# Kernel tuning notes

Hardware: AMD Instinct MI355X
Metric: run time of the kernel (lower is better)

## Reference

```python
import jax, jax.numpy as jnp
import numpy as np

D = 512      # d_model
H = 8        # nhead
HD = D // H  # head dim
L = 8        # axis-0 length (torch seq dim, batch_first=False)
S = 128      # axis-1 length (torch batch dim; relation-tensor axis)
NL = 3       # encoder layers
EPS = 1e-5


def setup_inputs() -> dict:
    key = jax.random.key(0)
    ks = jax.random.split(key, 16)
    w = lambda k, shape: jax.random.normal(k, shape, jnp.float32) * 0.02
    return {
        "x": jax.random.normal(ks[0], (L, S, D), jnp.float32),
        # stacked per-layer transformer params (leading dim = NL)
        "attn_in_w": w(ks[1], (NL, 3 * D, D)), "attn_in_b": jnp.zeros((NL, 3 * D), jnp.float32),
        "attn_out_w": w(ks[2], (NL, D, D)),    "attn_out_b": jnp.zeros((NL, D), jnp.float32),
        "ln1_w": jnp.ones((NL, D), jnp.float32), "ln1_b": jnp.zeros((NL, D), jnp.float32),
        "ln2_w": jnp.ones((NL, D), jnp.float32), "ln2_b": jnp.zeros((NL, D), jnp.float32),
        "ff1_w": w(ks[3], (NL, 4 * D, D)), "ff1_b": jnp.zeros((NL, 4 * D), jnp.float32),
        "ff2_w": w(ks[4], (NL, D, 4 * D)), "ff2_b": jnp.zeros((NL, D), jnp.float32),
        "fln_w": jnp.ones((D,), jnp.float32), "fln_b": jnp.zeros((D,), jnp.float32),
        # 4 projection MLPs stacked: 0=sub, 1=obj, 2=verb_sub, 3=verb_obj
        "mlp_w0": w(ks[5], (4, D, D)), "mlp_b0": jnp.zeros((4, D), jnp.float32),
        "mlp_w1": w(ks[6], (4, D, D)), "mlp_b1": jnp.zeros((4, D), jnp.float32),
        "mlp_w2": w(ks[7], (4, D, D)), "mlp_b2": jnp.zeros((4, D), jnp.float32),
    }


def _ln(x, w, b):
    m = jnp.mean(x, axis=-1, keepdims=True)
    v = jnp.mean(jnp.square(x - m), axis=-1, keepdims=True)
    return (x - m) * jax.lax.rsqrt(v + EPS) * w + b


def _mha(x, in_w, in_b, out_w, out_b):
    # x: (L, B, D); attention over axis 0 (torch batch_first=False semantics)
    l, b, _ = x.shape
    qkv = x @ in_w.T + in_b                      # (L, B, 3D)
    q, k, v = jnp.split(qkv, 3, axis=-1)
    q = q.reshape(l, b, H, HD)
    k = k.reshape(l, b, H, HD)
    v = v.reshape(l, b, H, HD)
    scores = jnp.einsum("lbhd,mbhd->bhlm", q, k) / jnp.sqrt(jnp.float32(HD))
    attn = jax.nn.softmax(scores, axis=-1)
    o = jnp.einsum("bhlm,mbhd->lbhd", attn, v).reshape(l, b, D)
    return o @ out_w.T + out_b


def _mlp(x, w0, b0, w1, b1, w2, b2):
    h = jax.nn.relu(x @ w0.T + b0)
    h = jax.nn.relu(h @ w1.T + b1)
    return h @ w2.T + b2


def _forward(x, attn_in_w, attn_in_b, attn_out_w, attn_out_b,
             ln1_w, ln1_b, ln2_w, ln2_b, ff1_w, ff1_b, ff2_w, ff2_b,
             fln_w, fln_b, mlp_w0, mlp_b0, mlp_w1, mlp_b1, mlp_w2, mlp_b2):
    # TransformerEncoder (post-norm, relu, no dropout at eval)
    h = x
    for i in range(NL):
        h = _ln(h + _mha(h, attn_in_w[i], attn_in_b[i], attn_out_w[i], attn_out_b[i]),
                ln1_w[i], ln1_b[i])
        ff = jax.nn.relu(h @ ff1_w[i].T + ff1_b[i]) @ ff2_w[i].T + ff2_b[i]
        h = _ln(h + ff, ln2_w[i], ln2_b[i])
    h = _ln(h, fln_w, fln_b)  # final encoder norm

    sub = _mlp(h, mlp_w0[0], mlp_b0[0], mlp_w1[0], mlp_b1[0], mlp_w2[0], mlp_b2[0])
    obj = _mlp(h, mlp_w0[1], mlp_b0[1], mlp_w1[1], mlp_b1[1], mlp_w2[1], mlp_b2[1])
    vsub = _mlp(h, mlp_w0[2], mlp_b0[2], mlp_w1[2], mlp_b1[2], mlp_w2[2], mlp_b2[2])
    vobj = _mlp(h, mlp_w0[3], mlp_b0[3], mlp_w1[3], mlp_b1[3], mlp_w2[3], mlp_b2[3])

    # sub.unsqueeze(1) * vsub.unsqueeze(2): (B0, S, S, D)
    sub4 = sub[:, None, :, :] * vsub[:, :, None, :]
    obj4 = obj[:, None, :, :] * vobj[:, :, None, :]
    # p_x = sub4 @ obj4.transpose(-2, -1): (B0, S, S, S)
    return jnp.einsum("bijd,bikd->bijk", sub4, obj4)


def reference(x, attn_in_w, attn_in_b, attn_out_w, attn_out_b,
              ln1_w, ln1_b, ln2_w, ln2_b, ff1_w, ff1_b, ff2_w, ff2_b,
              fln_w, fln_b, mlp_w0, mlp_b0, mlp_w1, mlp_b1, mlp_w2, mlp_b2):
    return _forward(x, attn_in_w, attn_in_b, attn_out_w, attn_out_b,
                    ln1_w, ln1_b, ln2_w, ln2_b, ff1_w, ff1_b, ff2_w, ff2_b,
                    fln_w, fln_b, mlp_w0, mlp_b0, mlp_w1, mlp_b1, mlp_w2, mlp_b2)
```

## Files before the change

### kernel.cpp

```cpp
#include <hip/hip_runtime.h>
#include <hip/hip_bf16.h>

#define DEV __device__ __forceinline__

typedef __attribute__((ext_vector_type(8))) short bf16x8;
typedef __attribute__((ext_vector_type(8))) unsigned short u16x8;
typedef __attribute__((ext_vector_type(4))) float f32x4;

DEV unsigned short f2bf(float f) {
  return __builtin_bit_cast(unsigned short, __float2bfloat16(f));
}
DEV float bf2f(unsigned short h) { return __uint_as_float(((unsigned int)h) << 16); }

DEV int swz(int row, int byteoff) { return row * 128 + (byteoff ^ ((row & 7) << 4)); }

__global__ void cvt_kernel(const float* __restrict__ src, unsigned short* __restrict__ dst,
                           float* __restrict__ dstf, int n) {
  long i = ((long)blockIdx.x * blockDim.x + threadIdx.x) * 8;
  long stride = (long)gridDim.x * blockDim.x * 8;
  for (; i < n; i += stride) {
    f32x4 a = *(const f32x4*)(src + i);
    f32x4 b = *(const f32x4*)(src + i + 4);
    u16x8 o;
    o[0] = f2bf(a[0]); o[1] = f2bf(a[1]); o[2] = f2bf(a[2]); o[3] = f2bf(a[3]);
    o[4] = f2bf(b[0]); o[5] = f2bf(b[1]); o[6] = f2bf(b[2]); o[7] = f2bf(b[3]);
    *(u16x8*)(dst + i) = o;
    if (dstf) { *(f32x4*)(dstf + i) = a; *(f32x4*)(dstf + i + 4) = b; }
  }
}

struct CvtJobs { const float* s[7]; unsigned short* d[7]; int n[7]; };
__global__ void cvtw_kernel(CvtJobs J) {
  const int seg = blockIdx.y;
  const float* __restrict__ src = J.s[seg];
  unsigned short* __restrict__ dst = J.d[seg];
  const int n = J.n[seg];
  long i = ((long)blockIdx.x * blockDim.x + threadIdx.x) * 8;
  long stride = (long)gridDim.x * blockDim.x * 8;
  for (; i < n; i += stride) {
    f32x4 a = *(const f32x4*)(src + i);
    f32x4 b = *(const f32x4*)(src + i + 4);
    u16x8 o;
    o[0] = f2bf(a[0]); o[1] = f2bf(a[1]); o[2] = f2bf(a[2]); o[3] = f2bf(a[3]);
    o[4] = f2bf(b[0]); o[5] = f2bf(b[1]); o[6] = f2bf(b[2]); o[7] = f2bf(b[3]);
    *(u16x8*)(dst + i) = o;
  }
}

template <int BM, int ACT, int WF32, int WBF>
__global__ __launch_bounds__(256) void gemm_kernel(
    const unsigned short* __restrict__ X, const unsigned short* __restrict__ Wt,
    const float* __restrict__ bias, float* Yf, unsigned short* __restrict__ Ybf,
    int M, int N, int K, long xbs, long wbs, long bbs, long ybs) {
  constexpr int CA = (BM * 64) / (256 * 8);
  constexpr int ABY = BM * 64 * 2;
  constexpr int BBY = 64 * 64 * 2;
  constexpr int MI = BM / 32;
  __shared__ __align__(16) char Asb[2 * ABY];
  __shared__ __align__(16) char Bsb[2 * BBY];
  const int t = threadIdx.x;
  const int bn = blockIdx.x, bm = blockIdx.y, bz = blockIdx.z;
  const unsigned short* Xp = X + (long)bz * xbs;
  const unsigned short* Wp = Wt + (long)bz * wbs;

  const int lane = t & 63, wv = t >> 6;
  const int wr = wv >> 1, wc = wv & 1;
  f32x4 acc[MI][2] = {};

  int rowA[CA], slotA[CA], rowB[2], slotB[2];
#pragma unroll
  for (int c = 0; c < CA; ++c) { int id = c * 256 + t; rowA[c] = id >> 3; slotA[c] = id & 7; }
#pragma unroll
  for (int c = 0; c < 2; ++c) { int id = c * 256 + t; rowB[c] = id >> 3; slotB[c] = id & 7; }

  u16x8 ra[CA], rb[2];
  auto load = [&](int kt) {
#pragma unroll
    for (int c = 0; c < CA; ++c)
      ra[c] = *(const u16x8*)(Xp + (long)(bm * BM + rowA[c]) * K + kt + slotA[c] * 8);
#pragma unroll
    for (int c = 0; c < 2; ++c)
      rb[c] = *(const u16x8*)(Wp + (long)(bn * 64 + rowB[c]) * K + kt + slotB[c] * 8);
  };
  auto store = [&](int cur) {
#pragma unroll
    for (int c = 0; c < CA; ++c)
      *(u16x8*)(Asb + cur * ABY + swz(rowA[c], slotA[c] * 16)) = ra[c];
#pragma unroll
    for (int c = 0; c < 2; ++c)
      *(u16x8*)(Bsb + cur * BBY + swz(rowB[c], slotB[c] * 16)) = rb[c];
  };

  const int NT = K >> 6;
  load(0);
  store(0);
  load(64);
  __syncthreads();
  for (int ki = 0; ki < NT; ++ki) {
    const int cur = ki & 1;
    if (ki + 1 < NT) store(cur ^ 1);
    if (ki + 2 < NT) load((ki + 2) << 6);
#pragma unroll
    for (int kk = 0; kk < 2; ++kk) {
      const int kb = kk * 64 + ((lane >> 4) << 4);
      bf16x8 af[MI], bfv[2];
#pragma unroll
      for (int mi = 0; mi < MI; ++mi)
        af[mi] = *(const bf16x8*)(Asb + cur * ABY + swz(wr * (MI * 16) + mi * 16 + (lane & 15), kb));
#pragma unroll
      for (int ni = 0; ni < 2; ++ni)
        bfv[ni] = *(const bf16x8*)(Bsb + cur * BBY + swz(wc * 32 + ni * 16 + (lane & 15), kb));
#pragma unroll
      for (int mi = 0; mi < MI; ++mi)
#pragma unroll
        for (int ni = 0; ni < 2; ++ni)
          acc[mi][ni] = __builtin_amdgcn_mfma_f32_16x16x32_bf16(af[mi], bfv[ni], acc[mi][ni], 0, 0, 0);
    }
    __syncthreads();
  }
#pragma unroll
  for (int ni = 0; ni < 2; ++ni) {
    const int n = bn * 64 + wc * 32 + ni * 16 + (lane & 15);
    const float bv = bias[(long)bz * bbs + n];
#pragma unroll
    for (int mi = 0; mi < MI; ++mi) {
#pragma unroll
      for (int rr = 0; rr < 4; ++rr) {
        const int gm = bm * BM + wr * (MI * 16) + mi * 16 + ((lane >> 4) << 2) + rr;
        float v = acc[mi][ni][rr] + bv;
        if (ACT == 1) v = fmaxf(v, 0.f);
        const long o = (long)bz * ybs + (long)gm * N + n;
        if (WF32) Yf[o] = v;
        if (WBF) Ybf[o] = f2bf(v);
      }
    }
  }
}

__global__ __launch_bounds__(256) void attn_kernel(const unsigned short* __restrict__ qkv,
                                                   unsigned short* __restrict__ o) {
  __shared__ float P[512];
  const int s = blockIdx.x;
  const int t = threadIdx.x;
#pragma unroll
  for (int rep = 0; rep < 2; ++rep) {
    const int idx = t + rep * 256;
    const int h = idx >> 6, l = (idx >> 3) & 7, m = idx & 7;
    const unsigned short* qp = qkv + (long)(l * 128 + s) * 1536 + h * 64;
    const unsigned short* kp = qkv + (long)(m * 128 + s) * 1536 + 512 + h * 64;
    float acc = 0.f;
#pragma unroll
    for (int c = 0; c < 64; c += 8) {
      u16x8 q8 = *(const u16x8*)(qp + c);
      u16x8 k8 = *(const u16x8*)(kp + c);
#pragma unroll
      for (int j = 0; j < 8; ++j) acc += bf2f(q8[j]) * bf2f(k8[j]);
    }
    P[idx] = acc * 0.125f;
  }
  __syncthreads();
  if (t < 64) {
    const int base = t * 8;
    float mx = -1e30f;
#pragma unroll
    for (int m = 0; m < 8; ++m) mx = fmaxf(mx, P[base + m]);
    float e[8], sum = 0.f;
#pragma unroll
    for (int m = 0; m < 8; ++m) { e[m] = expf(P[base + m] - mx); sum += e[m]; }
    const float inv = 1.f / sum;
#pragma unroll
    for (int m = 0; m < 8; ++m) P[base + m] = e[m] * inv;
  }
  __syncthreads();
#pragma unroll
  for (int rep = 0; rep < 16; ++rep) {
    const int idx = t + rep * 256;
    const int d = idx & 63, h = (idx >> 6) & 7, l = idx >> 9;
    float acc = 0.f;
#pragma unroll
    for (int m = 0; m < 8; ++m)
      acc += P[h * 64 + l * 8 + m] * bf2f(qkv[(long)(m * 128 + s) * 1536 + 1024 + h * 64 + d]);
    o[(long)(l * 128 + s) * 512 + h * 64 + d] = f2bf(acc);
  }
}

template <int RES, int WF32>
__global__ __launch_bounds__(256) void ln_kernel(const float* a, const float* res,
                                                 const float* __restrict__ w,
                                                 const float* __restrict__ bb, float* hf,
                                                 unsigned short* __restrict__ hbf) {
  __shared__ float red[8];
  const int row = blockIdx.x, t = threadIdx.x;
  const long base = (long)row * 512;
  float x0 = a[base + t], x1 = a[base + t + 256];
  if (RES) { x0 += res[base + t]; x1 += res[base + t + 256]; }
  float s = x0 + x1;
#pragma unroll
  for (int msk = 32; msk; msk >>= 1) s += __shfl_xor(s, msk, 64);
  if ((t & 63) == 0) red[t >> 6] = s;
  __syncthreads();
  const float mean = (red[0] + red[1] + red[2] + red[3]) * (1.f / 512.f);
  const float d0 = x0 - mean, d1 = x1 - mean;
  float v = d0 * d0 + d1 * d1;
#pragma unroll
  for (int msk = 32; msk; msk >>= 1) v += __shfl_xor(v, msk, 64);
  if ((t & 63) == 0) red[4 + (t >> 6)] = v;
  __syncthreads();
  const float var = (red[4] + red[5] + red[6] + red[7]) * (1.f / 512.f);
  const float inv = rsqrtf(var + 1e-5f);
  const float o0 = d0 * inv * w[t] + bb[t];
  const float o1 = d1 * inv * w[t + 256] + bb[t + 256];
  if (WF32) { hf[base + t] = o0; hf[base + t + 256] = o1; }
  hbf[base + t] = f2bf(o0);
  hbf[base + t + 256] = f2bf(o1);
}

__global__ __launch_bounds__(256) void phasec_kernel(const float* __restrict__ subp,
                                                     const unsigned short* __restrict__ objbf,
                                                     const float* __restrict__ vsub,
                                                     const float* __restrict__ vobj,
                                                     float* __restrict__ out) {
  constexpr int ABY = 128 * 64 * 2;
  __shared__ __align__(16) char Asb[2 * ABY];
  __shared__ __align__(16) char Bsb[2 * ABY];
  __shared__ float Wl[512];
  const int t = threadIdx.x;
  const int i = blockIdx.x, b = blockIdx.y;
  const long base_bi = ((long)b * 128 + i) * 512;
  for (int d = t; d < 512; d += 256) Wl[d] = vsub[base_bi + d] * vobj[base_bi + d];

  const int lane = t & 63, wv = t >> 6;
  const int wr = wv >> 1, wc = wv & 1;
  f32x4 acc[4][4] = {};

  int row[4], slot[4];
#pragma unroll
  for (int c = 0; c < 4; ++c) { int id = c * 256 + t; row[c] = id >> 3; slot[c] = id & 7; }

  f32x4 fa[4][2];
  u16x8 rb[4];
  auto load = [&](int kt) {
#pragma unroll
    for (int c = 0; c < 4; ++c) {
      const long g = ((long)b * 128 + row[c]) * 512 + kt + slot[c] * 8;
      fa[c][0] = *(const f32x4*)(subp + g);
      fa[c][1] = *(const f32x4*)(subp + g + 4);
      rb[c] = *(const u16x8*)(objbf + g);
    }
  };
  auto store = [&](int cur, int ktd) {
#pragma unroll
    for (int c = 0; c < 4; ++c) {
      const float* wp = Wl + ktd + slot[c] * 8;
      f32x4 w0 = *(const f32x4*)wp;
      f32x4 w1 = *(const f32x4*)(wp + 4);
      u16x8 oa;
      oa[0] = f2bf(fa[c][0][0] * w0[0]); oa[1] = f2bf(fa[c][0][1] * w0[1]);
      oa[2] = f2bf(fa[c][0][2] * w0[2]); oa[3] = f2bf(fa[c][0][3] * w0[3]);
      oa[4] = f2bf(fa[c][1][0] * w1[0]); oa[5] = f2bf(fa[c][1][1] * w1[1]);
      oa[6] = f2bf(fa[c][1][2] * w1[2]); oa[7] = f2bf(fa[c][1][3] * w1[3]);
      *(u16x8*)(Asb + cur * ABY + swz(row[c], slot[c] * 16)) = oa;
      *(u16x8*)(Bsb + cur * ABY + swz(row[c], slot[c] * 16)) = rb[c];
    }
  };

  __syncthreads();
  load(0);
  store(0, 0);
  load(64);
  __syncthreads();
  for (int ki = 0; ki < 8; ++ki) {
    const int cur = ki & 1;
    if (ki + 1 < 8) store(cur ^ 1, (ki + 1) * 64);
    if (ki + 2 < 8) load((ki + 2) * 64);
#pragma unroll
    for (int kk = 0; kk < 2; ++kk) {
      const int kb = kk * 64 + ((lane >> 4) << 4);
      bf16x8 af[4], bfv[4];
#pragma unroll
      for (int mi = 0; mi < 4; ++mi)
        af[mi] = *(const bf16x8*)(Asb + cur * ABY + swz(wr * 64 + mi * 16 + (lane & 15), kb));
#pragma unroll
      for (int ni = 0; ni < 4; ++ni)
        bfv[ni] = *(const bf16x8*)(Bsb + cur * ABY + swz(wc * 64 + ni * 16 + (lane & 15), kb));
#pragma unroll
      for (int mi = 0; mi < 4; ++mi)
#pragma unroll
        for (int ni = 0; ni < 4; ++ni)
          acc[mi][ni] = __builtin_amdgcn_mfma_f32_16x16x32_bf16(af[mi], bfv[ni], acc[mi][ni], 0, 0, 0);
    }
    __syncthreads();
  }
  float* ob = out + ((long)b * 128 + i) * 128 * 128;
#pragma unroll
  for (int mi = 0; mi < 4; ++mi) {
#pragma unroll
    for (int rr = 0; rr < 4; ++rr) {
      const int j = wr * 64 + mi * 16 + ((lane >> 4) << 2) + rr;
      float* orow = ob + (long)j * 128 + wc * 64 + (lane & 15);
#pragma unroll
      for (int ni = 0; ni < 4; ++ni) orow[ni * 16] = acc[mi][ni][rr];
    }
  }
}

extern "C" void kernel_launch(void* const* d_in, const int* in_sizes, int n_in, void* d_out,
                              int out_size, void* d_ws, size_t ws_size, hipStream_t stream) {
  const float* x          = (const float*)d_in[0];
  const float* attn_in_w  = (const float*)d_in[1];
  const float* attn_in_b  = (const float*)d_in[2];
  const float* attn_out_w = (const float*)d_in[3];
  const float* attn_out_b = (const float*)d_in[4];
  const float* ln1_w = (const float*)d_in[5];
  const float* ln1_b = (const float*)d_in[6];
  const float* ln2_w = (const float*)d_in[7];
  const float* ln2_b = (const float*)d_in[8];
  const float* ff1_w = (const float*)d_in[9];
  const float* ff1_b = (const float*)d_in[10];
  const float* ff2_w = (const float*)d_in[11];
  const float* ff2_b = (const float*)d_in[12];
  const float* fln_w = (const float*)d_in[13];
  const float* fln_b = (const float*)d_in[14];
  const float* mlp_w0 = (const float*)d_in[15];
  const float* mlp_b0 = (const float*)d_in[16];
  const float* mlp_w1 = (const float*)d_in[17];
  const float* mlp_b1 = (const float*)d_in[18];
  const float* mlp_w2 = (const float*)d_in[19];
  const float* mlp_b2 = (const float*)d_in[20];
  float* out = (float*)d_out;
  (void)in_sizes; (void)n_in; (void)out_size; (void)ws_size;

  char* ws = (char*)d_ws;
  size_t off = 0;
  auto alloc = [&](size_t bytes) -> void* {
    void* p = (void*)(ws + off);
    off += (bytes + 255) & ~(size_t)255;
    return p;
  };
  unsigned short* wq  = (unsigned short*)alloc((size_t)3 * 1536 * 512 * 2);
  unsigned short* wo  = (unsigned short*)alloc((size_t)3 * 512 * 512 * 2);
  unsigned short* wf1 = (unsigned short*)alloc((size_t)3 * 2048 * 512 * 2);
  unsigned short* wf2 = (unsigned short*)alloc((size_t)3 * 512 * 2048 * 2);
  unsigned short* wm0 = (unsigned short*)alloc((size_t)4 * 512 * 512 * 2);
  unsigned short* wm1 = (unsigned short*)alloc((size_t)4 * 512 * 512 * 2);
  unsigned short* wm2 = (unsigned short*)alloc((size_t)4 * 512 * 512 * 2);
  float* h            = (float*)alloc((size_t)1024 * 512 * 4);
  unsigned short* hbf = (unsigned short*)alloc((size_t)1024 * 512 * 2);
  unsigned short* t1  = (unsigned short*)alloc((size_t)1024 * 2048 * 2);
  float* t2           = (float*)alloc((size_t)1024 * 512 * 4);
  unsigned short* ao  = (unsigned short*)alloc((size_t)1024 * 512 * 2);
  unsigned short* z1  = (unsigned short*)alloc((size_t)4 * 1024 * 512 * 2);
  unsigned short* z2  = (unsigned short*)alloc((size_t)4 * 1024 * 512 * 2);
  float* hf4          = (float*)alloc((size_t)4 * 1024 * 512 * 4);
  unsigned short* hb4 = (unsigned short*)alloc((size_t)4 * 1024 * 512 * 2);

  CvtJobs J;
  J.s[0] = attn_in_w;  J.d[0] = wq;  J.n[0] = 3 * 1536 * 512;
  J.s[1] = attn_out_w; J.d[1] = wo;  J.n[1] = 3 * 512 * 512;
  J.s[2] = ff1_w;      J.d[2] = wf1; J.n[2] = 3 * 2048 * 512;
  J.s[3] = ff2_w;      J.d[3] = wf2; J.n[3] = 3 * 512 * 2048;
  J.s[4] = mlp_w0;     J.d[4] = wm0; J.n[4] = 4 * 512 * 512;
  J.s[5] = mlp_w1;     J.d[5] = wm1; J.n[5] = 4 * 512 * 512;
  J.s[6] = mlp_w2;     J.d[6] = wm2; J.n[6] = 4 * 512 * 512;
  cvtw_kernel<<<dim3(512, 7), 256, 0, stream>>>(J);
  cvt_kernel<<<256, 256, 0, stream>>>(x, hbf, h, 1024 * 512);

  for (int i = 0; i < 3; ++i) {
    gemm_kernel<64, 0, 0, 1><<<dim3(24, 16, 1), 256, 0, stream>>>(
        hbf, wq + (long)i * 1536 * 512, attn_in_b + i * 1536, nullptr, t1, 1024, 1536, 512, 0, 0, 0, 0);
    attn_kernel<<<128, 256, 0, stream>>>(t1, ao);
    gemm_kernel<32, 0, 1, 0><<<dim3(8, 32, 1), 256, 0, stream>>>(
        ao, wo + (long)i * 512 * 512, attn_out_b + i * 512, t2, nullptr, 1024, 512, 512, 0, 0, 0, 0);
    ln_kernel<1, 1><<<1024, 256, 0, stream>>>(t2, h, ln1_w + i * 512, ln1_b + i * 512, h, hbf);
    gemm_kernel<64, 1, 0, 1><<<dim3(32, 16, 1), 256, 0, stream>>>(
        hbf, wf1 + (long)i * 2048 * 512, ff1_b + i * 2048, nullptr, t1, 1024, 2048, 512, 0, 0, 0, 0);
    gemm_kernel<32, 0, 1, 0><<<dim3(8, 32, 1), 256, 0, stream>>>(
        t1, wf2 + (long)i * 512 * 2048, ff2_b + i * 512, t2, nullptr, 1024, 512, 2048, 0, 0, 0, 0);
    ln_kernel<1, 1><<<1024, 256, 0, stream>>>(t2, h, ln2_w + i * 512, ln2_b + i * 512, h, hbf);
  }
  ln_kernel<0, 0><<<1024, 256, 0, stream>>>(h, nullptr, fln_w, fln_b, h, hbf);

  gemm_kernel<32, 1, 0, 1><<<dim3(8, 32, 4), 256, 0, stream>>>(
      hbf, wm0, mlp_b0, nullptr, z1, 1024, 512, 512, 0, 512 * 512, 512, 1024 * 512);
  gemm_kernel<32, 1, 0, 1><<<dim3(8, 32, 4), 256, 0, stream>>>(
      z1, wm1, mlp_b1, nullptr, z2, 1024, 512, 512, 1024 * 512, 512 * 512, 512, 1024 * 512);
  gemm_kernel<32, 0, 1, 1><<<dim3(8, 32, 4), 256, 0, stream>>>(
      z2, wm2, mlp_b2, hf4, hb4, 1024, 512, 512, 1024 * 512, 512 * 512, 512, 1024 * 512);

  phasec_kernel<<<dim3(128, 8), 256, 0, stream>>>(
      hf4, hb4 + 1 * 1024 * 512, hf4 + 2L * 1024 * 512, hf4 + 3L * 1024 * 512, out);
}
```

Before: 379.6 us.

## Fuse encoder and MLP stages into one persistent kernel with grid barriers

Replaces the roughly 25 separate GEMM, attention and layernorm launches with a single persistent 256-block kernel. Stages are separated by a software grid barrier built on atomics, and GEMM tiles are distributed round-robin across blocks. It also folds the residual add into the GEMM epilogue, rewrites layernorm as one wave per row with a single pass, merges the input conversion into the weight-conversion launch, and stages the phasec output through shared memory for vectorized stores. The aim is to cut launch and tail overhead, at the cost of needing all blocks co-resident for the barrier and of fewer blocks per GEMM stage.

```diff
diff --git a/kernel.cpp b/kernel.cpp
--- a/kernel.cpp
+++ b/kernel.cpp
@@ -5,7 +5,11 @@
 
 typedef __attribute__((ext_vector_type(8))) short bf16x8;
 typedef __attribute__((ext_vector_type(8))) unsigned short u16x8;
+typedef __attribute__((ext_vector_type(4))) unsigned short u16x4;
 typedef __attribute__((ext_vector_type(4))) float f32x4;
+
+#define GRID 256
+#define BLOCK 512
 
 DEV unsigned short f2bf(float f) {
   return __builtin_bit_cast(unsigned short, __float2bfloat16(f));
@@ -14,8 +18,30 @@
 
 DEV int swz(int row, int byteoff) { return row * 128 + (byteoff ^ ((row & 7) << 4)); }
 
-__global__ void cvt_kernel(const float* __restrict__ src, unsigned short* __restrict__ dst,
-                           float* __restrict__ dstf, int n) {
+DEV void gridbar(unsigned* cnt, unsigned* gen) {
+  __syncthreads();
+  if (threadIdx.x == 0) {
+    __threadfence();
+    unsigned g = __hip_atomic_load(gen, __ATOMIC_RELAXED, __HIP_MEMORY_SCOPE_AGENT);
+    unsigned old = __hip_atomic_fetch_add(cnt, 1u, __ATOMIC_ACQ_REL, __HIP_MEMORY_SCOPE_AGENT);
+    if (old == GRID - 1) {
+      __hip_atomic_store(cnt, 0u, __ATOMIC_RELAXED, __HIP_MEMORY_SCOPE_AGENT);
+      __hip_atomic_fetch_add(gen, 1u, __ATOMIC_ACQ_REL, __HIP_MEMORY_SCOPE_AGENT);
+    } else {
+      while (__hip_atomic_load(gen, __ATOMIC_ACQUIRE, __HIP_MEMORY_SCOPE_AGENT) == g)
+        __builtin_amdgcn_s_sleep(2);
+    }
+  }
+  __syncthreads();
+}
+
+struct CvtJobs { const float* s[8]; unsigned short* d[8]; float* df[8]; int n[8]; };
+__global__ void cvtw_kernel(CvtJobs J) {
+  const int seg = blockIdx.y;
+  const float* __restrict__ src = J.s[seg];
+  unsigned short* __restrict__ dst = J.d[seg];
+  float* __restrict__ dstf = J.df[seg];
+  const int n = J.n[seg];
   long i = ((long)blockIdx.x * blockDim.x + threadIdx.x) * 8;
   long stride = (long)gridDim.x * blockDim.x * 8;
   for (; i < n; i += stride) {
@@ -29,123 +55,143 @@
   }
 }
 
-struct CvtJobs { const float* s[7]; unsigned short* d[7]; int n[7]; };
-__global__ void cvtw_kernel(CvtJobs J) {
-  const int seg = blockIdx.y;
-  const float* __restrict__ src = J.s[seg];
-  unsigned short* __restrict__ dst = J.d[seg];
-  const int n = J.n[seg];
-  long i = ((long)blockIdx.x * blockDim.x + threadIdx.x) * 8;
-  long stride = (long)gridDim.x * blockDim.x * 8;
-  for (; i < n; i += stride) {
-    f32x4 a = *(const f32x4*)(src + i);
-    f32x4 b = *(const f32x4*)(src + i + 4);
-    u16x8 o;
-    o[0] = f2bf(a[0]); o[1] = f2bf(a[1]); o[2] = f2bf(a[2]); o[3] = f2bf(a[3]);
-    o[4] = f2bf(b[0]); o[5] = f2bf(b[1]); o[6] = f2bf(b[2]); o[7] = f2bf(b[3]);
-    *(u16x8*)(dst + i) = o;
-  }
-}
-
-template <int BM, int ACT, int WF32, int WBF>
-__global__ __launch_bounds__(256) void gemm_kernel(
-    const unsigned short* __restrict__ X, const unsigned short* __restrict__ Wt,
-    const float* __restrict__ bias, float* Yf, unsigned short* __restrict__ Ybf,
-    int M, int N, int K, long xbs, long wbs, long bbs, long ybs) {
-  constexpr int CA = (BM * 64) / (256 * 8);
-  constexpr int ABY = BM * 64 * 2;
-  constexpr int BBY = 64 * 64 * 2;
-  constexpr int MI = BM / 32;
-  __shared__ __align__(16) char Asb[2 * ABY];
-  __shared__ __align__(16) char Bsb[2 * BBY];
-  const int t = threadIdx.x;
-  const int bn = blockIdx.x, bm = blockIdx.y, bz = blockIdx.z;
-  const unsigned short* Xp = X + (long)bz * xbs;
-  const unsigned short* Wp = Wt + (long)bz * wbs;
-
+template <int BM, int BN, int ACT, int OUTF32, int OUTBF, int RES>
+DEV void gemm_stage(char* SM, int bid, int t,
+                    const unsigned short* __restrict__ X, const unsigned short* __restrict__ W,
+                    const float* __restrict__ bias, const float* __restrict__ res,
+                    float* __restrict__ Yf, unsigned short* __restrict__ Ybf,
+                    int M, int N, int K, int NB, long xbs, long wbs, long bbs, long ybs) {
+  constexpr int ABY = BM * 64 * 2, BBY = BN * 64 * 2;
+  constexpr int MI = BM / 32, NI = BN / 64;
+  constexpr int CB = (BN * 8) / BLOCK;
+  char* Asb = SM;
+  char* Bsb = SM + 2 * ABY;
+  const int lane = t & 63, wv = t >> 6, wr = wv >> 2, wc = wv & 3;
+  const int tilesN = N / BN, tpb = (M / BM) * tilesN;
+  const int ntile = NB * tpb;
+  const int rowA = t >> 3, slotA = t & 7;
+  int rowB[CB], slotB[CB];
+#pragma unroll
+  for (int c = 0; c < CB; ++c) { int id = c * BLOCK + t; rowB[c] = id >> 3; slotB[c] = id & 7; }
+
+  for (int tile = bid; tile < ntile; tile += GRID) {
+    const int z = tile / tpb, rem = tile % tpb, tm = rem / tilesN, tn = rem % tilesN;
+    const unsigned short* Xp = X + (long)z * xbs + (long)tm * BM * K;
+    const unsigned short* Wp = W + (long)z * wbs + (long)tn * BN * K;
+    f32x4 acc[MI][NI];
+#pragma unroll
+    for (int mi = 0; mi < MI; ++mi)
+#pragma unroll
+      for (int ni = 0; ni < NI; ++ni) acc[mi][ni] = f32x4{0.f, 0.f, 0.f, 0.f};
+
+    u16x8 ra, rbv[CB];
+    auto load = [&](int kt) {
+      if (BM * 8 == BLOCK || t < BM * 8)
+        ra = *(const u16x8*)(Xp + (long)rowA * K + kt + slotA * 8);
+#pragma unroll
+      for (int c = 0; c < CB; ++c)
+        rbv[c] = *(const u16x8*)(Wp + (long)rowB[c] * K + kt + slotB[c] * 8);
+    };
+    auto store = [&](int cur) {
+      if (BM * 8 == BLOCK || t < BM * 8)
+        *(u16x8*)(Asb + cur * ABY + swz(rowA, slotA * 16)) = ra;
+#pragma unroll
+      for (int c = 0; c < CB; ++c)
+        *(u16x8*)(Bsb + cur * BBY + swz(rowB[c], slotB[c] * 16)) = rbv[c];
+    };
+
+    const int NT = K >> 6;
+    load(0);
+    store(0);
+    load(64);
+    __syncthreads();
+    for (int ki = 0; ki < NT; ++ki) {
+      const int cur = ki & 1;
+      if (ki + 1 < NT) store(cur ^ 1);
+      if (ki + 2 < NT) load((ki + 2) << 6);
+#pragma unroll
+      for (int kk = 0; kk < 2; ++kk) {
+        const int kb = kk * 64 + ((lane >> 4) << 4);
+        bf16x8 af[MI], bfv[NI];
+#pragma unroll
+        for (int mi = 0; mi < MI; ++mi)
+          af[mi] = *(const bf16x8*)(Asb + cur * ABY + swz(wr * (BM / 2) + mi * 16 + (lane & 15), kb));
+#pragma unroll
+        for (int ni = 0; ni < NI; ++ni)
+          bfv[ni] = *(const bf16x8*)(Bsb + cur * BBY + swz(wc * (BN / 4) + ni * 16 + (lane & 15), kb));
+#pragma unroll
+        for (int mi = 0; mi < MI; ++mi)
+#pragma unroll
+          for (int ni = 0; ni < NI; ++ni)
+            acc[mi][ni] = __builtin_amdgcn_mfma_f32_16x16x32_bf16(af[mi], bfv[ni], acc[mi][ni], 0, 0, 0);
+      }
+      __syncthreads();
+    }
+#pragma unroll
+    for (int ni = 0; ni < NI; ++ni) {
+      const int gn = tn * BN + wc * (BN / 4) + ni * 16 + (lane & 15);
+      const float bv = bias[(long)z * bbs + gn];
+#pragma unroll
+      for (int mi = 0; mi < MI; ++mi) {
+#pragma unroll
+        for (int rr = 0; rr < 4; ++rr) {
+          const int gm = tm * BM + wr * (BM / 2) + mi * 16 + ((lane >> 4) << 2) + rr;
+          float v = acc[mi][ni][rr] + bv;
+          if (RES) v += res[(long)gm * N + gn];
+          if (ACT) v = fmaxf(v, 0.f);
+          const long o = (long)z * ybs + (long)gm * N + gn;
+          if (OUTF32) Yf[o] = v;
+          if (OUTBF) Ybf[o] = f2bf(v);
+        }
+      }
+    }
+    __syncthreads();
+  }
+}
+
+DEV void ln_stage(int bid, int t, const float* __restrict__ in,
+                  const float* __restrict__ g, const float* __restrict__ b,
+                  float* __restrict__ outf, unsigned short* __restrict__ outbf, int writef) {
   const int lane = t & 63, wv = t >> 6;
-  const int wr = wv >> 1, wc = wv & 1;
-  f32x4 acc[MI][2] = {};
-
-  int rowA[CA], slotA[CA], rowB[2], slotB[2];
-#pragma unroll
-  for (int c = 0; c < CA; ++c) { int id = c * 256 + t; rowA[c] = id >> 3; slotA[c] = id & 7; }
-#pragma unroll
-  for (int c = 0; c < 2; ++c) { int id = c * 256 + t; rowB[c] = id >> 3; slotB[c] = id & 7; }
-
-  u16x8 ra[CA], rb[2];
-  auto load = [&](int kt) {
-#pragma unroll
-    for (int c = 0; c < CA; ++c)
-      ra[c] = *(const u16x8*)(Xp + (long)(bm * BM + rowA[c]) * K + kt + slotA[c] * 8);
-#pragma unroll
-    for (int c = 0; c < 2; ++c)
-      rb[c] = *(const u16x8*)(Wp + (long)(bn * 64 + rowB[c]) * K + kt + slotB[c] * 8);
-  };
-  auto store = [&](int cur) {
-#pragma unroll
-    for (int c = 0; c < CA; ++c)
-      *(u16x8*)(Asb + cur * ABY + swz(rowA[c], slotA[c] * 16)) = ra[c];
-#pragma unroll
-    for (int c = 0; c < 2; ++c)
-      *(u16x8*)(Bsb + cur * BBY + swz(rowB[c], slotB[c] * 16)) = rb[c];
-  };
-
-  const int NT = K >> 6;
-  load(0);
-  store(0);
-  load(64);
-  __syncthreads();
-  for (int ki = 0; ki < NT; ++ki) {
-    const int cur = ki & 1;
-    if (ki + 1 < NT) store(cur ^ 1);
-    if (ki + 2 < NT) load((ki + 2) << 6);
-#pragma unroll
-    for (int kk = 0; kk < 2; ++kk) {
-      const int kb = kk * 64 + ((lane >> 4) << 4);
-      bf16x8 af[MI], bfv[2];
-#pragma unroll
-      for (int mi = 0; mi < MI; ++mi)
-        af[mi] = *(const bf16x8*)(Asb + cur * ABY + swz(wr * (MI * 16) + mi * 16 + (lane & 15), kb));
-#pragma unroll
-      for (int ni = 0; ni < 2; ++ni)
-        bfv[ni] = *(const bf16x8*)(Bsb + cur * BBY + swz(wc * 32 + ni * 16 + (lane & 15), kb));
-#pragma unroll
-      for (int mi = 0; mi < MI; ++mi)
-#pragma unroll
-        for (int ni = 0; ni < 2; ++ni)
-          acc[mi][ni] = __builtin_amdgcn_mfma_f32_16x16x32_bf16(af[mi], bfv[ni], acc[mi][ni], 0, 0, 0);
-    }
-    __syncthreads();
-  }
-#pragma unroll
-  for (int ni = 0; ni < 2; ++ni) {
-    const int n = bn * 64 + wc * 32 + ni * 16 + (lane & 15);
-    const float bv = bias[(long)bz * bbs + n];
-#pragma unroll
-    for (int mi = 0; mi < MI; ++mi) {
-#pragma unroll
-      for (int rr = 0; rr < 4; ++rr) {
-        const int gm = bm * BM + wr * (MI * 16) + mi * 16 + ((lane >> 4) << 2) + rr;
-        float v = acc[mi][ni][rr] + bv;
-        if (ACT == 1) v = fmaxf(v, 0.f);
-        const long o = (long)bz * ybs + (long)gm * N + n;
-        if (WF32) Yf[o] = v;
-        if (WBF) Ybf[o] = f2bf(v);
-      }
-    }
-  }
-}
-
-__global__ __launch_bounds__(256) void attn_kernel(const unsigned short* __restrict__ qkv,
-                                                   unsigned short* __restrict__ o) {
-  __shared__ float P[512];
-  const int s = blockIdx.x;
-  const int t = threadIdx.x;
-#pragma unroll
-  for (int rep = 0; rep < 2; ++rep) {
-    const int idx = t + rep * 256;
-    const int h = idx >> 6, l = (idx >> 3) & 7, m = idx & 7;
+  if (wv < 4) {
+    const int row = bid * 4 + wv;
+    const float* p = in + (long)row * 512 + lane * 8;
+    f32x4 a = *(const f32x4*)p;
+    f32x4 c = *(const f32x4*)(p + 4);
+    float s = a[0] + a[1] + a[2] + a[3] + c[0] + c[1] + c[2] + c[3];
+    float q = a[0]*a[0] + a[1]*a[1] + a[2]*a[2] + a[3]*a[3] +
+              c[0]*c[0] + c[1]*c[1] + c[2]*c[2] + c[3]*c[3];
+#pragma unroll
+    for (int msk = 32; msk; msk >>= 1) { s += __shfl_xor(s, msk, 64); q += __shfl_xor(q, msk, 64); }
+    const float mean = s * (1.f / 512.f);
+    const float var = q * (1.f / 512.f) - mean * mean;
+    const float inv = rsqrtf(var + 1e-5f);
+    const float* gp = g + lane * 8;
+    const float* bp = b + lane * 8;
+    float o[8];
+#pragma unroll
+    for (int j = 0; j < 4; ++j) o[j] = (a[j] - mean) * inv * gp[j] + bp[j];
+#pragma unroll
+    for (int j = 0; j < 4; ++j) o[4 + j] = (c[j] - mean) * inv * gp[4 + j] + bp[4 + j];
+    if (writef) {
+      f32x4 w0 = {o[0], o[1], o[2], o[3]}, w1 = {o[4], o[5], o[6], o[7]};
+      *(f32x4*)(outf + (long)row * 512 + lane * 8) = w0;
+      *(f32x4*)(outf + (long)row * 512 + lane * 8 + 4) = w1;
+    }
+    u16x8 ob;
+#pragma unroll
+    for (int j = 0; j < 8; ++j) ob[j] = f2bf(o[j]);
+    *(u16x8*)(outbf + (long)row * 512 + lane * 8) = ob;
+  }
+}
+
+DEV void attn_stage(char* SM, int bid, int t, const unsigned short* __restrict__ qkv,
+                    unsigned short* __restrict__ ao) {
+  float* P = (float*)SM;
+  const int s = bid >> 1, hg = bid & 1;
+  if (t < 256) {
+    const int hh = t >> 6, l = (t >> 3) & 7, m = t & 7;
+    const int h = hg * 4 + hh;
     const unsigned short* qp = qkv + (long)(l * 128 + s) * 1536 + h * 64;
     const unsigned short* kp = qkv + (long)(m * 128 + s) * 1536 + 512 + h * 64;
     float acc = 0.f;
@@ -156,10 +202,10 @@
 #pragma unroll
       for (int j = 0; j < 8; ++j) acc += bf2f(q8[j]) * bf2f(k8[j]);
     }
-    P[idx] = acc * 0.125f;
-  }
-  __syncthreads();
-  if (t < 64) {
+    P[t] = acc * 0.125f;
+  }
+  __syncthreads();
+  if (t < 32) {
     const int base = t * 8;
     float mx = -1e30f;
 #pragma unroll
@@ -172,47 +218,71 @@
     for (int m = 0; m < 8; ++m) P[base + m] = e[m] * inv;
   }
   __syncthreads();
-#pragma unroll
-  for (int rep = 0; rep < 16; ++rep) {
-    const int idx = t + rep * 256;
-    const int d = idx & 63, h = (idx >> 6) & 7, l = idx >> 9;
-    float acc = 0.f;
-#pragma unroll
-    for (int m = 0; m < 8; ++m)
-      acc += P[h * 64 + l * 8 + m] * bf2f(qkv[(long)(m * 128 + s) * 1536 + 1024 + h * 64 + d]);
-    o[(long)(l * 128 + s) * 512 + h * 64 + d] = f2bf(acc);
-  }
-}
-
-template <int RES, int WF32>
-__global__ __launch_bounds__(256) void ln_kernel(const float* a, const float* res,
-                                                 const float* __restrict__ w,
-                                                 const float* __restrict__ bb, float* hf,
-                                                 unsigned short* __restrict__ hbf) {
-  __shared__ float red[8];
-  const int row = blockIdx.x, t = threadIdx.x;
-  const long base = (long)row * 512;
-  float x0 = a[base + t], x1 = a[base + t + 256];
-  if (RES) { x0 += res[base + t]; x1 += res[base + t + 256]; }
-  float s = x0 + x1;
-#pragma unroll
-  for (int msk = 32; msk; msk >>= 1) s += __shfl_xor(s, msk, 64);
-  if ((t & 63) == 0) red[t >> 6] = s;
-  __syncthreads();
-  const float mean = (red[0] + red[1] + red[2] + red[3]) * (1.f / 512.f);
-  const float d0 = x0 - mean, d1 = x1 - mean;
-  float v = d0 * d0 + d1 * d1;
-#pragma unroll
-  for (int msk = 32; msk; msk >>= 1) v += __shfl_xor(v, msk, 64);
-  if ((t & 63) == 0) red[4 + (t >> 6)] = v;
-  __syncthreads();
-  const float var = (red[4] + red[5] + red[6] + red[7]) * (1.f / 512.f);
-  const float inv = rsqrtf(var + 1e-5f);
-  const float o0 = d0 * inv * w[t] + bb[t];
-  const float o1 = d1 * inv * w[t + 256] + bb[t + 256];
-  if (WF32) { hf[base + t] = o0; hf[base + t + 256] = o1; }
-  hbf[base + t] = f2bf(o0);
-  hbf[base + t + 256] = f2bf(o1);
+  const int l = t >> 6, hh = (t >> 4) & 3, d4 = (t & 15) * 4;
+  const int h = hg * 4 + hh;
+  float o[4] = {0.f, 0.f, 0.f, 0.f};
+#pragma unroll
+  for (int m = 0; m < 8; ++m) {
+    const float p = P[hh * 64 + l * 8 + m];
+    const unsigned short* vp = qkv + (long)(m * 128 + s) * 1536 + 1024 + h * 64 + d4;
+#pragma unroll
+    for (int dd = 0; dd < 4; ++dd) o[dd] += p * bf2f(vp[dd]);
+  }
+  u16x4 pk;
+#pragma unroll
+  for (int dd = 0; dd < 4; ++dd) pk[dd] = f2bf(o[dd]);
+  *(u16x4*)(ao + (long)(l * 128 + s) * 512 + h * 64 + d4) = pk;
+}
+
+struct Params {
+  const float *attn_in_b, *attn_out_b, *ln1_w, *ln1_b, *ln2_w, *ln2_b,
+              *ff1_b, *ff2_b, *fln_w, *fln_b, *mlp_b0, *mlp_b1, *mlp_b2;
+  const unsigned short *wq, *wo, *wf1, *wf2, *wm0, *wm1, *wm2;
+  float *h, *t2, *hf4;
+  unsigned short *hbf, *t1, *ao, *z1, *z2, *hb4;
+  unsigned* sync;
+};
+
+__global__ __launch_bounds__(BLOCK, 1) void fused_kernel(Params P) {
+  __shared__ __align__(16) char SM[49152];
+  const int bid = blockIdx.x, t = threadIdx.x;
+  unsigned* cnt = P.sync;
+  unsigned* gen = P.sync + 1;
+
+  for (int L = 0; L < 3; ++L) {
+    gemm_stage<64, 128, 0, 0, 1, 0>(SM, bid, t, P.hbf, P.wq + (long)L * 1536 * 512,
+                                    P.attn_in_b + L * 1536, nullptr, nullptr, P.t1,
+                                    1024, 1536, 512, 1, 0, 0, 0, 0);
+    gridbar(cnt, gen);
+    attn_stage(SM, bid, t, P.t1, P.ao);
+    gridbar(cnt, gen);
+    gemm_stage<32, 64, 0, 1, 0, 1>(SM, bid, t, P.ao, P.wo + (long)L * 512 * 512,
+                                   P.attn_out_b + L * 512, P.h, P.t2, nullptr,
+                                   1024, 512, 512, 1, 0, 0, 0, 0);
+    gridbar(cnt, gen);
+    ln_stage(bid, t, P.t2, P.ln1_w + L * 512, P.ln1_b + L * 512, P.h, P.hbf, 1);
+    gridbar(cnt, gen);
+    gemm_stage<64, 128, 1, 0, 1, 0>(SM, bid, t, P.hbf, P.wf1 + (long)L * 2048 * 512,
+                                    P.ff1_b + L * 2048, nullptr, nullptr, P.t1,
+                                    1024, 2048, 512, 1, 0, 0, 0, 0);
+    gridbar(cnt, gen);
+    gemm_stage<32, 64, 0, 1, 0, 1>(SM, bid, t, P.t1, P.wf2 + (long)L * 512 * 2048,
+                                   P.ff2_b + L * 512, P.h, P.t2, nullptr,
+                                   1024, 512, 2048, 1, 0, 0, 0, 0);
+    gridbar(cnt, gen);
+    ln_stage(bid, t, P.t2, P.ln2_w + L * 512, P.ln2_b + L * 512, P.h, P.hbf, 1);
+    gridbar(cnt, gen);
+  }
+  ln_stage(bid, t, P.h, P.fln_w, P.fln_b, nullptr, P.hbf, 0);
+  gridbar(cnt, gen);
+  gemm_stage<64, 128, 1, 0, 1, 0>(SM, bid, t, P.hbf, P.wm0, P.mlp_b0, nullptr, nullptr, P.z1,
+                                  1024, 512, 512, 4, 0, 512 * 512, 512, 1024 * 512);
+  gridbar(cnt, gen);
+  gemm_stage<64, 128, 1, 0, 1, 0>(SM, bid, t, P.z1, P.wm1, P.mlp_b1, nullptr, nullptr, P.z2,
+                                  1024, 512, 512, 4, 1024 * 512, 512 * 512, 512, 1024 * 512);
+  gridbar(cnt, gen);
+  gemm_stage<64, 128, 0, 1, 1, 0>(SM, bid, t, P.z2, P.wm2, P.mlp_b2, nullptr, P.hf4, P.hb4,
+                                  1024, 512, 512, 4, 1024 * 512, 512 * 512, 512, 1024 * 512);
 }
 
 __global__ __launch_bounds__(256) void phasec_kernel(const float* __restrict__ subp,
@@ -221,9 +291,10 @@
                                                      const float* __restrict__ vobj,
                                                      float* __restrict__ out) {
   constexpr int ABY = 128 * 64 * 2;
-  __shared__ __align__(16) char Asb[2 * ABY];
-  __shared__ __align__(16) char Bsb[2 * ABY];
-  __shared__ float Wl[512];
+  __shared__ __align__(16) char SMEM[67584];
+  char* Asb = SMEM;
+  char* Bsb = SMEM + 2 * ABY;
+  float* Wl = (float*)(SMEM + 4 * ABY);
   const int t = threadIdx.x;
   const int i = blockIdx.x, b = blockIdx.y;
   const long base_bi = ((long)b * 128 + i) * 512;
@@ -291,16 +362,24 @@
     }
     __syncthreads();
   }
-  float* ob = out + ((long)b * 128 + i) * 128 * 128;
-#pragma unroll
-  for (int mi = 0; mi < 4; ++mi) {
+  float* C = (float*)SMEM;
+#pragma unroll
+  for (int mi = 0; mi < 4; ++mi)
 #pragma unroll
     for (int rr = 0; rr < 4; ++rr) {
       const int j = wr * 64 + mi * 16 + ((lane >> 4) << 2) + rr;
-      float* orow = ob + (long)j * 128 + wc * 64 + (lane & 15);
-#pragma unroll
-      for (int ni = 0; ni < 4; ++ni) orow[ni * 16] = acc[mi][ni][rr];
-    }
+      float* crow = C + j * 132 + wc * 64 + (lane & 15);
+#pragma unroll
+      for (int ni = 0; ni < 4; ++ni) crow[ni * 16] = acc[mi][ni][rr];
+    }
+  __syncthreads();
+  float* ob = out + ((long)b * 128 + i) * 128 * 128;
+  const int cc = (t & 31) * 4, jb = (t >> 5) * 16;
+#pragma unroll
+  for (int q = 0; q < 16; ++q) {
+    const int j = jb + q;
+    f32x4 v = *(const f32x4*)(C + j * 132 + cc);
+    *(f32x4*)(ob + (long)j * 128 + cc) = v;
   }
 }
 
@@ -337,6 +416,7 @@
     off += (bytes + 255) & ~(size_t)255;
     return p;
   };
+  unsigned* syncp     = (unsigned*)alloc(256);
   unsigned short* wq  = (unsigned short*)alloc((size_t)3 * 1536 * 512 * 2);
   unsigned short* wo  = (unsigned short*)alloc((size_t)3 * 512 * 512 * 2);
   unsigned short* wf1 = (unsigned short*)alloc((size_t)3 * 2048 * 512 * 2);
@@ -354,7 +434,10 @@
   float* hf4          = (float*)alloc((size_t)4 * 1024 * 512 * 4);
   unsigned short* hb4 = (unsigned short*)alloc((size_t)4 * 1024 * 512 * 2);
 
+  hipMemsetAsync(syncp, 0, 8, stream);
+
   CvtJobs J;
+  for (int k = 0; k < 8; ++k) J.df[k] = nullptr;
   J.s[0] = attn_in_w;  J.d[0] = wq;  J.n[0] = 3 * 1536 * 512;
   J.s[1] = attn_out_w; J.d[1] = wo;  J.n[1] = 3 * 512 * 512;
   J.s[2] = ff1_w;      J.d[2] = wf1; J.n[2] = 3 * 2048 * 512;
@@ -362,30 +445,20 @@
   J.s[4] = mlp_w0;     J.d[4] = wm0; J.n[4] = 4 * 512 * 512;
   J.s[5] = mlp_w1;     J.d[5] = wm1; J.n[5] = 4 * 512 * 512;
   J.s[6] = mlp_w2;     J.d[6] = wm2; J.n[6] = 4 * 512 * 512;
-  cvtw_kernel<<<dim3(512, 7), 256, 0, stream>>>(J);
-  cvt_kernel<<<256, 256, 0, stream>>>(x, hbf, h, 1024 * 512);
-
-  for (int i = 0; i < 3; ++i) {
-    gemm_kernel<64, 0, 0, 1><<<dim3(24, 16, 1), 256, 0, stream>>>(
-        hbf, wq + (long)i * 1536 * 512, attn_in_b + i * 1536, nullptr, t1, 1024, 1536, 512, 0, 0, 0, 0);
-    attn_kernel<<<128, 256, 0, stream>>>(t1, ao);
-    gemm_kernel<32, 0, 1, 0><<<dim3(8, 32, 1), 256, 0, stream>>>(
-        ao, wo + (long)i * 512 * 512, attn_out_b + i * 512, t2, nullptr, 1024, 512, 512, 0, 0, 0, 0);
-    ln_kernel<1, 1><<<1024, 256, 0, stream>>>(t2, h, ln1_w + i * 512, ln1_b + i * 512, h, hbf);
-    gemm_kernel<64, 1, 0, 1><<<dim3(32, 16, 1), 256, 0, stream>>>(
-        hbf, wf1 + (long)i * 2048 * 512, ff1_b + i * 2048, nullptr, t1, 1024, 2048, 512, 0, 0, 0, 0);
-    gemm_kernel<32, 0, 1, 0><<<dim3(8, 32, 1), 256, 0, stream>>>(
-        t1, wf2 + (long)i * 512 * 2048, ff2_b + i * 512, t2, nullptr, 1024, 512, 2048, 0, 0, 0, 0);
-    ln_kernel<1, 1><<<1024, 256, 0, stream>>>(t2, h, ln2_w + i * 512, ln2_b + i * 512, h, hbf);
-  }
-  ln_kernel<0, 0><<<1024, 256, 0, stream>>>(h, nullptr, fln_w, fln_b, h, hbf);
-
-  gemm_kernel<32, 1, 0, 1><<<dim3(8, 32, 4), 256, 0, stream>>>(
-      hbf, wm0, mlp_b0, nullptr, z1, 1024, 512, 512, 0, 512 * 512, 512, 1024 * 512);
-  gemm_kernel<32, 1, 0, 1><<<dim3(8, 32, 4), 256, 0, stream>>>(
-      z1, wm1, mlp_b1, nullptr, z2, 1024, 512, 512, 1024 * 512, 512 * 512, 512, 1024 * 512);
-  gemm_kernel<32, 0, 1, 1><<<dim3(8, 32, 4), 256, 0, stream>>>(
-      z2, wm2, mlp_b2, hf4, hb4, 1024, 512, 512, 1024 * 512, 512 * 512, 512, 1024 * 512);
+  J.s[7] = x;          J.d[7] = hbf; J.n[7] = 1024 * 512; J.df[7] = h;
+  cvtw_kernel<<<dim3(512, 8), 256, 0, stream>>>(J);
+
+  Params P;
+  P.attn_in_b = attn_in_b; P.attn_out_b = attn_out_b;
+  P.ln1_w = ln1_w; P.ln1_b = ln1_b; P.ln2_w = ln2_w; P.ln2_b = ln2_b;
+  P.ff1_b = ff1_b; P.ff2_b = ff2_b; P.fln_w = fln_w; P.fln_b = fln_b;
+  P.mlp_b0 = mlp_b0; P.mlp_b1 = mlp_b1; P.mlp_b2 = mlp_b2;
+  P.wq = wq; P.wo = wo; P.wf1 = wf1; P.wf2 = wf2;
+  P.wm0 = wm0; P.wm1 = wm1; P.wm2 = wm2;
+  P.h = h; P.t2 = t2; P.hf4 = hf4;
+  P.hbf = hbf; P.t1 = t1; P.ao = ao; P.z1 = z1; P.z2 = z2; P.hb4 = hb4;
+  P.sync = syncp;
+  fused_kernel<<<GRID, BLOCK, 0, stream>>>(P);
 
   phasec_kernel<<<dim3(128, 8), 256, 0, stream>>>(
       hf4, hb4 + 1 * 1024 * 512, hf4 + 2L * 1024 * 512, hf4 + 3L * 1024 * 512, out);
```

After: 1.261 ms. 232% more time.
